# Kernel optimization log

Hardware: AMD Instinct MI355X
Metric: run time of the kernel (lower is better)

The kernel has to match this reference:

```python
import jax, jax.numpy as jnp
import numpy as np

B, S, E = 2, 2048, 2048
H, KVH, D = 16, 4, 128
GROUPS = H // KVH
WINDOW = 1024
CAP = 50.0
ROPE_BASE = 10000.0
RMS_EPS = 1e-6
LN_EPS = 1e-5

def setup_inputs() -> dict:
    key = jax.random.key(0)
    ks = jax.random.split(key, 5)
    return {
        "x": jax.random.normal(ks[0], (B, S, E), jnp.float32),
        "Wq": jax.random.normal(ks[1], (E, E), jnp.float32) * (1.0 / np.sqrt(E)),
        "Wk": jax.random.normal(ks[2], (KVH * D, E), jnp.float32) * (1.0 / np.sqrt(E)),
        "Wv": jax.random.normal(ks[3], (KVH * D, E), jnp.float32) * (1.0 / np.sqrt(E)),
        "Wo": jax.random.normal(ks[4], (E, E), jnp.float32) * (1.0 / np.sqrt(E * H)),
        "q_norm_w": jnp.ones((D,), jnp.float32),
        "k_norm_w": jnp.ones((D,), jnp.float32),
        "ln_gamma": jnp.ones((E,), jnp.float32),
        "ln_beta": jnp.zeros((E,), jnp.float32),
    }

def _rmsnorm(t, w):
    # normalize over last (head) dim
    var = jnp.mean(jnp.square(t), axis=-1, keepdims=True)
    return t * jax.lax.rsqrt(var + RMS_EPS) * w

def _rope(t):
    # t: [B, h, S, D]; rotate-half RoPE
    half = D // 2
    inv_freq = 1.0 / (ROPE_BASE ** (jnp.arange(0, D, 2, dtype=jnp.float32) / D))  # [D/2]
    ang = jnp.arange(S, dtype=jnp.float32)[:, None] * inv_freq[None, :]  # [S, D/2]
    cos = jnp.concatenate([jnp.cos(ang), jnp.cos(ang)], axis=-1)  # [S, D]
    sin = jnp.concatenate([jnp.sin(ang), jnp.sin(ang)], axis=-1)
    t1, t2 = t[..., :half], t[..., half:]
    rot = jnp.concatenate([-t2, t1], axis=-1)
    return t * cos + rot * sin

def reference(x, Wq, Wk, Wv, Wo, q_norm_w, k_norm_w, ln_gamma, ln_beta):
    b, s, _ = x.shape
    q = (x @ Wq.T).reshape(b, s, H, D).transpose(0, 2, 1, 3)    # [B,H,S,D]
    k = (x @ Wk.T).reshape(b, s, KVH, D).transpose(0, 2, 1, 3)  # [B,KVH,S,D]
    v = (x @ Wv.T).reshape(b, s, KVH, D).transpose(0, 2, 1, 3)
    # QK-RMSNorm (Gemma/PaLM2 style), then RoPE
    q = _rope(_rmsnorm(q, q_norm_w))
    k = _rope(_rmsnorm(k, k_norm_w))
    # GQA: repeat KV heads to match query heads
    k = jnp.repeat(k, GROUPS, axis=1)  # [B,H,S,D]
    v = jnp.repeat(v, GROUPS, axis=1)
    scores = jnp.einsum('bhqd,bhkd->bhqk', q, k) / jnp.sqrt(jnp.asarray(D, x.dtype))
    # tanh logit softcap (Gemma2)
    scores = CAP * jnp.tanh(scores / CAP)
    # causal + sliding-window mask: attend to j with 0 <= i-j < WINDOW
    i = jnp.arange(s)[:, None]
    j = jnp.arange(s)[None, :]
    mask = (j <= i) & ((i - j) < WINDOW)  # [S,S]
    neg = jnp.finfo(scores.dtype).min
    scores = jnp.where(mask[None, None], scores, neg)
    attn = jax.nn.softmax(scores, axis=-1)
    out = jnp.einsum('bhqk,bhkd->bhqd', attn, v)  # [B,H,S,D]
    out = out.transpose(0, 2, 1, 3).reshape(b, s, E) @ Wo.T
    # residual + LayerNorm (post-norm)
    y = x + out
    mu = jnp.mean(y, axis=-1, keepdims=True)
    var = jnp.var(y, axis=-1, keepdims=True)
    return (y - mu) * jax.lax.rsqrt(var + LN_EPS) * ln_gamma + ln_beta
```

## Files before the change

### kernel.cpp

```cpp
#include <hip/hip_runtime.h>
#include <stdint.h>

typedef __attribute__((ext_vector_type(8))) short short8;
typedef __attribute__((ext_vector_type(4))) float f32x4;
typedef unsigned short u16;
typedef unsigned int u32;

#define NTOK 4096
#define E 2048
#define S 2048
#define NH 16
#define NKVH 4
#define HD 128
#define NQKV 3072

__device__ __forceinline__ float bf2f(u16 u) {
    return __uint_as_float(((u32)u) << 16);
}
__device__ __forceinline__ u16 f2bf(float f) {
    u32 u = __float_as_uint(f);
    u32 r = (u + 0x7fffu + ((u >> 16) & 1u)) >> 16;
    return (u16)r;
}
__device__ __forceinline__ void gload_lds16(const u16* g, u16* l) {
    __builtin_amdgcn_global_load_lds(
        (const __attribute__((address_space(1))) unsigned int*)(g),
        (__attribute__((address_space(3))) unsigned int*)(l), 16, 0, 0);
}

__global__ void cast5(const float* __restrict__ x, const float* __restrict__ wq,
                      const float* __restrict__ wk, const float* __restrict__ wv,
                      const float* __restrict__ wo,
                      u16* __restrict__ xb, u16* __restrict__ wqkvb,
                      u16* __restrict__ wob) {
    int i = blockIdx.x * 256 + threadIdx.x;
    const float* s; u16* d; int rel;
    if (i < 2097152)      { s = x;  d = xb;  rel = i; }
    else if (i < 3145728) { s = wq; d = wqkvb; rel = i - 2097152; }
    else if (i < 3407872) { s = wk; d = wqkvb + 4194304; rel = i - 3145728; }
    else if (i < 3670016) { s = wv; d = wqkvb + 5242880; rel = i - 3407872; }
    else                  { s = wo; d = wob; rel = i - 3670016; }
    float4 v = *(const float4*)(s + (size_t)rel * 4);
    ushort4 o;
    o.x = f2bf(v.x); o.y = f2bf(v.y); o.z = f2bf(v.z); o.w = f2bf(v.w);
    *(ushort4*)(d + (size_t)rel * 4) = o;
}

#define LADDR(row, ko) ((row) * 64 + ((ko) ^ (((row) & 7) << 3)))
#define GSB   __builtin_amdgcn_sched_barrier(0)
#define GBAR  __builtin_amdgcn_s_barrier()
#define LGKM0 do { asm volatile("s_waitcnt lgkmcnt(0)" ::: "memory"); GSB; } while (0)
#define MIDBAR do { GSB; GBAR; LGKM0; } while (0)
#define ENDBAR do { __builtin_amdgcn_s_setprio(0); GSB; GBAR; } while (0)

__device__ __forceinline__ void stage1(u16* lds, const u16* g, int row0,
                                       int kt, int K, int tid) {
    const int rr = tid >> 3;
    const int chunk = (tid & 7) ^ (rr & 7);
    gload_lds16(g + (size_t)(row0 + rr) * K + kt + chunk * 8,
                lds + (row0 + (tid >> 6) * 8) * 64);
}

__global__ __launch_bounds__(512, 2)
void gemm_qkv(const u16* __restrict__ A, const u16* __restrict__ Bt,
              float* __restrict__ C, int M, int N, int K) {
    __shared__ u16 As2[2 * 8192];
    __shared__ u16 Bs2[2 * 12288];
    const int tid = threadIdx.x;
    const int w = tid >> 6, lane = tid & 63;
    const int lr = lane & 15, quad = lane >> 4;
    const int qo = quad * 8;
    const int wr = w >> 2, wc = w & 3;
    const int am = wr * 64;
    const int bn = wc * 48;

    const int nbx = N / 192;
    int wg = blockIdx.x;
    {
        const int nwg = gridDim.x;
        const int q = nwg >> 3, r = nwg & 7;
        const int xcd = wg & 7, loc = wg >> 3;
        wg = (xcd < r ? xcd * (q + 1) : r * (q + 1) + (xcd - r) * q) + loc;
    }
    const int n0 = (wg % nbx) * 192;
    const int m0 = (wg / nbx) * 128;

    const u16* gA = A + (size_t)m0 * K;
    const u16* gB = Bt + (size_t)n0 * K;
    const int nt = K >> 6;

    f32x4 acc[4][3];
#pragma unroll
    for (int mi = 0; mi < 4; mi++)
#pragma unroll
        for (int ni = 0; ni < 3; ni++)
            acc[mi][ni] = (f32x4){0.f, 0.f, 0.f, 0.f};

    short8 af[4][2], bf[3][2];

    stage1(As2, gA, 0, 0, K, tid);
    stage1(As2, gA, 64, 0, K, tid);
#pragma unroll
    for (int r = 0; r < 3; r++) stage1(Bs2, gB, r * 64, 0, K, tid);
    if (nt > 1) {
        stage1(As2 + 8192, gA, 0, 64, K, tid);
        stage1(As2 + 8192, gA, 64, 64, K, tid);
        stage1(Bs2 + 12288, gB, 0, 64, K, tid);
        stage1(Bs2 + 12288, gB, 64, 64, K, tid);
        asm volatile("s_waitcnt vmcnt(4)" ::: "memory");
    } else {
        asm volatile("s_waitcnt vmcnt(0)" ::: "memory");
    }
    GSB; GBAR;

    for (int t = 0; t < nt; ++t) {
        const int pb = t & 1;
        u16* Ap = As2 + pb * 8192;
        u16* Bp = Bs2 + pb * 12288;
        u16* Bn = Bs2 + (pb ^ 1) * 12288;
        const int kt1 = (t + 1) << 6, kt2 = (t + 2) << 6;

#pragma unroll
        for (int mi = 0; mi < 4; mi++)
#pragma unroll
            for (int kk = 0; kk < 2; kk++)
                af[mi][kk] = *(const short8*)&Ap[LADDR(am + mi * 16 + lr, kk * 32 + qo)];
#pragma unroll
        for (int ni = 0; ni < 3; ni++)
#pragma unroll
            for (int kk = 0; kk < 2; kk++)
                bf[ni][kk] = *(const short8*)&Bp[LADDR(bn + ni * 16 + lr, kk * 32 + qo)];
        if (t + 1 < nt) stage1(Bn, gB, 128, kt1, K, tid);
        GSB; GBAR; LGKM0;
        __builtin_amdgcn_s_setprio(1);
#pragma unroll
        for (int mi = 0; mi < 4; mi++)
#pragma unroll
            for (int ni = 0; ni < 3; ni++)
#pragma unroll
                for (int kk = 0; kk < 2; kk++)
                    acc[mi][ni] = __builtin_amdgcn_mfma_f32_16x16x32_bf16(
                        af[mi][kk], bf[ni][kk], acc[mi][ni], 0, 0, 0);
        __builtin_amdgcn_s_setprio(0);
        if (t + 2 < nt) {
            stage1(Ap, gA, 0, kt2, K, tid);
            stage1(Ap, gA, 64, kt2, K, tid);
            stage1(Bp, gB, 0, kt2, K, tid);
            stage1(Bp, gB, 64, kt2, K, tid);
        }
        if (t + 2 >= nt) {
            asm volatile("s_waitcnt vmcnt(0)" ::: "memory");
        } else {
            asm volatile("s_waitcnt vmcnt(4)" ::: "memory");
        }
        GSB; GBAR;
    }

#pragma unroll
    for (int mi = 0; mi < 4; mi++)
#pragma unroll
        for (int ni = 0; ni < 3; ni++) {
            const int row = m0 + am + mi * 16 + quad * 4;
            const int col = n0 + bn + ni * 16 + lr;
            f32x4 v = acc[mi][ni];
            C[(size_t)(row + 0) * N + col] = v[0];
            C[(size_t)(row + 1) * N + col] = v[1];
            C[(size_t)(row + 2) * N + col] = v[2];
            C[(size_t)(row + 3) * N + col] = v[3];
        }
}

__device__ __forceinline__ void stageA(u16* lds, const u16* g, int ldsrow0,
                                       int g0, int g1, int kt, int K, int tid) {
    const int rr = tid >> 3;
    const int chunk = (tid & 7) ^ (rr & 7);
    const int w8 = (tid >> 6) * 8;
    gload_lds16(g + (size_t)(g0 + rr) * K + kt + chunk * 8,
                lds + (ldsrow0 + w8) * 64);
    gload_lds16(g + (size_t)(g1 + rr) * K + kt + chunk * 8,
                lds + (ldsrow0 + 64 + w8) * 64);
}
__device__ __forceinline__ void stageB(u16* lds, const u16* g, int ldsrow0,
                                       int b0, int b1, int kt, int K, int tid) {
    const int rr = tid >> 3;
    const int grow = (rr & 31) | ((rr & 32) << 1);
    const int chunk = (tid & 7) ^ (rr & 7);
    const int w8 = (tid >> 6) * 8;
    gload_lds16(g + (size_t)(b0 + grow) * K + kt + chunk * 8,
                lds + (ldsrow0 + w8) * 64);
    gload_lds16(g + (size_t)(b1 + grow) * K + kt + chunk * 8,
                lds + (ldsrow0 + 64 + w8) * 64);
}

__global__ __launch_bounds__(512, 2)
void gemm8p(const u16* __restrict__ A, const u16* __restrict__ Bt,
            float* __restrict__ C, int M, int N, int K, int ksz, int nsplit) {
    __shared__ u16 As[2 * 16384];
    __shared__ u16 Bs[2 * 16384];
    const int tid = threadIdx.x;
    const int w = tid >> 6, lane = tid & 63;
    const int lr = lane & 15, quad = lane >> 4;
    const int qo = quad * 8;
    const int wm = (w >> 2) * 128, wn = (w & 3) * 64;
    const int wmh = (w >> 2) * 64, wnq = (w & 3) * 32;

    const int nbx = N >> 8;
    int wg = blockIdx.x;
    {
        const int nwg = gridDim.x;
        const int q = nwg >> 3, r = nwg & 7;
        const int xcd = wg & 7, loc = wg >> 3;
        wg = (xcd < r ? xcd * (q + 1) : r * (q + 1) + (xcd - r) * q) + loc;
    }
    int split = 0;
    if (nsplit == 2) { split = wg & 1; wg >>= 1; }
    const int n0 = (wg % nbx) << 8;
    const int m0 = (wg / nbx) << 8;

    const u16* gA = A + (size_t)m0 * K + split * ksz;
    const u16* gB = Bt + (size_t)n0 * K + split * ksz;
    C += (size_t)split * M * N;
    const int nt = ksz >> 6;

    f32x4 acc[8][4];
#pragma unroll
    for (int mi = 0; mi < 8; mi++)
#pragma unroll
        for (int ni = 0; ni < 4; ni++)
            acc[mi][ni] = (f32x4){0.f, 0.f, 0.f, 0.f};

    short8 alo[4][2], ahi[4][2], blo[2][2], bhi[2][2];

    stageA(As, gA, 0, 0, 128, 0, K, tid);
    stageB(Bs, gB, 0, 0, 128, 0, K, tid);
    stageB(Bs, gB, 128, 32, 160, 0, K, tid);
    stageA(As, gA, 128, 64, 192, 0, K, tid);
    if (nt > 1) {
        stageA(As + 16384, gA, 0, 0, 128, 64, K, tid);
        stageB(Bs + 16384, gB, 0, 0, 128, 64, K, tid);
        stageB(Bs + 16384, gB, 128, 32, 160, 64, K, tid);
        asm volatile("s_waitcnt vmcnt(6)" ::: "memory");
    } else {
        asm volatile("s_waitcnt vmcnt(0)" ::: "memory");
    }
    GSB; GBAR;

    for (int t = 0; t < nt; ++t) {
        const int pb = t & 1;
        u16* Ap = As + pb * 16384;
        u16* Bp = Bs + pb * 16384;
        u16* An = As + (pb ^ 1) * 16384;
        const int kt1 = (t + 1) << 6, kt2 = (t + 2) << 6;

#pragma unroll
        for (int mi = 0; mi < 4; mi++)
#pragma unroll
            for (int kk = 0; kk < 2; kk++)
                alo[mi][kk] = *(const short8*)&Ap[LADDR(wmh + mi * 16 + lr, kk * 32 + qo)];
#pragma unroll
        for (int ni = 0; ni < 2; ni++)
#pragma unroll
            for (int kk = 0; kk < 2; kk++)
                blo[ni][kk] = *(const short8*)&Bp[LADDR(wnq + ni * 16 + lr, kk * 32 + qo)];
        if (t + 1 < nt) stageA(An, gA, 128, 64, 192, kt1, K, tid);
        MIDBAR;
        __builtin_amdgcn_s_setprio(1);
#pragma unroll
        for (int mi = 0; mi < 4; mi++)
#pragma unroll
            for (int ni = 0; ni < 2; ni++)
#pragma unroll
                for (int kk = 0; kk < 2; kk++)
                    acc[mi][ni] = __builtin_amdgcn_mfma_f32_16x16x32_bf16(
                        alo[mi][kk], blo[ni][kk], acc[mi][ni], 0, 0, 0);
        ENDBAR;

#pragma unroll
        for (int ni = 0; ni < 2; ni++)
#pragma unroll
            for (int kk = 0; kk < 2; kk++)
                bhi[ni][kk] = *(const short8*)&Bp[LADDR(128 + wnq + ni * 16 + lr, kk * 32 + qo)];
        if (t + 2 < nt) stageA(Ap, gA, 0, 0, 128, kt2, K, tid);
        MIDBAR;
        __builtin_amdgcn_s_setprio(1);
#pragma unroll
        for (int mi = 0; mi < 4; mi++)
#pragma unroll
            for (int ni = 0; ni < 2; ni++)
#pragma unroll
                for (int kk = 0; kk < 2; kk++)
                    acc[mi][ni + 2] = __builtin_amdgcn_mfma_f32_16x16x32_bf16(
                        alo[mi][kk], bhi[ni][kk], acc[mi][ni + 2], 0, 0, 0);
        ENDBAR;

#pragma unroll
        for (int mi = 0; mi < 4; mi++)
#pragma unroll
            for (int kk = 0; kk < 2; kk++)
                ahi[mi][kk] = *(const short8*)&Ap[LADDR(128 + wmh + mi * 16 + lr, kk * 32 + qo)];
        if (t + 2 < nt) stageB(Bp, gB, 0, 0, 128, kt2, K, tid);
        MIDBAR;
        __builtin_amdgcn_s_setprio(1);
#pragma unroll
        for (int mi = 0; mi < 4; mi++)
#pragma unroll
            for (int ni = 0; ni < 2; ni++)
#pragma unroll
                for (int kk = 0; kk < 2; kk++)
                    acc[mi + 4][ni + 2] = __builtin_amdgcn_mfma_f32_16x16x32_bf16(
                        ahi[mi][kk], bhi[ni][kk], acc[mi + 4][ni + 2], 0, 0, 0);
        ENDBAR;

        if (t + 2 < nt) stageB(Bp, gB, 128, 32, 160, kt2, K, tid);
        __builtin_amdgcn_s_setprio(1);
#pragma unroll
        for (int mi = 0; mi < 4; mi++)
#pragma unroll
            for (int ni = 0; ni < 2; ni++)
#pragma unroll
                for (int kk = 0; kk < 2; kk++)
                    acc[mi + 4][ni] = __builtin_amdgcn_mfma_f32_16x16x32_bf16(
                        ahi[mi][kk], blo[ni][kk], acc[mi + 4][ni], 0, 0, 0);
        __builtin_amdgcn_s_setprio(0);
        if (t + 2 >= nt) {
            asm volatile("s_waitcnt vmcnt(0)" ::: "memory");
        } else {
            asm volatile("s_waitcnt vmcnt(6)" ::: "memory");
        }
        GSB; GBAR;
    }

#pragma unroll
    for (int mi = 0; mi < 8; mi++)
#pragma unroll
        for (int ni = 0; ni < 4; ni++) {
            const int row = m0 + wm + mi * 16 + quad * 4;
            const int col = n0 + wn + ni * 16 + lr;
            f32x4 v = acc[mi][ni];
            C[(size_t)(row + 0) * N + col] = v[0];
            C[(size_t)(row + 1) * N + col] = v[1];
            C[(size_t)(row + 2) * N + col] = v[2];
            C[(size_t)(row + 3) * N + col] = v[3];
        }
}

#define LDT 65
#define RMSBLKS 20480
__global__ __launch_bounds__(256)
void prep(const float* __restrict__ qkv,
          const float* __restrict__ qw, const float* __restrict__ kw,
          u16* __restrict__ qdst, u16* __restrict__ kdst, u16* __restrict__ vdst) {
    __shared__ u16 Ts[128 * LDT];
    if (blockIdx.x < RMSBLKS) {
        int p = blockIdx.x * 4 + (threadIdx.x >> 6);
        int lane = threadIdx.x & 63;
        const float* src; const float* w; u16* dst; int HH;
        if (p < NTOK * NH) { src = qkv; w = qw; dst = qdst; HH = NH; }
        else { p -= NTOK * NH; src = qkv + 2048; w = kw; dst = kdst; HH = NKVH; }
        int n = p / HH;
        int h = p - n * HH;
        int b = n >> 11;
        int s = n & 2047;
        const float* row = src + (size_t)n * NQKV + h * HD;
        float t1 = row[lane];
        float t2 = row[lane + 64];
        float ss = t1 * t1 + t2 * t2;
#pragma unroll
        for (int o = 1; o < 64; o <<= 1) ss += __shfl_xor(ss, o);
        float r = rsqrtf(ss * (1.f / 128.f) + 1e-6f);
        float a1 = t1 * r * w[lane];
        float a2 = t2 * r * w[lane + 64];
        float freq = expf(lane * -0.14391156831212787f);
        float ang = (float)s * freq;
        float sn, cs;
        sincosf(ang, &sn, &cs);
        float o1 = a1 * cs - a2 * sn;
        float o2 = a2 * cs + a1 * sn;
        size_t base = (((size_t)(b * HH + h)) * S + s) * HD;
        dst[base + lane] = f2bf(o1);
        dst[base + 64 + lane] = f2bf(o2);
    } else {
        const int idx = blockIdx.x - RMSBLKS;
        const int t = threadIdx.x;
        const int s0 = (idx & 31) * 64;
        const int kh = (idx >> 5) & 3;
        const int b = idx >> 7;
        const float* base = qkv + ((size_t)(b * S + s0)) * NQKV + 2560 + kh * HD;
#pragma unroll
        for (int i = 0; i < 8; i++) {
            int ii = i * 256 + t;
            int r = ii >> 5, c4 = (ii & 31) * 4;
            float4 v = *(const float4*)(base + (size_t)r * NQKV + c4);
            Ts[(c4 + 0) * LDT + r] = f2bf(v.x);
            Ts[(c4 + 1) * LDT + r] = f2bf(v.y);
            Ts[(c4 + 2) * LDT + r] = f2bf(v.z);
            Ts[(c4 + 3) * LDT + r] = f2bf(v.w);
        }
        __syncthreads();
        u16* obase = vdst + ((size_t)(b * NKVH + kh) * HD) * S + s0;
#pragma unroll
        for (int i = 0; i < 4; i++) {
            int ii = i * 256 + t;
            int d = ii >> 3, s8 = (ii & 7) * 8;
            const u16* row = &Ts[d * LDT + s8];
            short8 o;
#pragma unroll
            for (int j = 0; j < 8; j++) o[j] = (short)row[j];
            *(short8*)(obase + (size_t)d * S + s8) = o;
        }
    }
}

#define KSX(key, cb) ((key) * 128 + ((((cb) ^ ((key) & 15))) * 8))
#define VSX(d, cb)   ((d) * 64 + ((((cb) ^ ((d) & 7))) * 8))
#define PSX(row, cb) ((row) * 64 + ((((cb) ^ ((row) & 7))) * 8))
#define QBLK 64

__global__ __launch_bounds__(256, 4)
void attn_mfma(const u16* __restrict__ qa, const u16* __restrict__ ka,
               const u16* __restrict__ vt, u16* __restrict__ out) {
    __shared__ u16 Ks[64 * 128];
    __shared__ u16 Vs[128 * 64];
    __shared__ u16 Ps[64 * 64];
    const int tid = threadIdx.x;
    const int w = tid >> 6, lane = tid & 63;
    const int lr = lane & 15, quad = lane >> 4;

    const int bid = blockIdx.x;
    const int g = bid >> 8, p = bid & 255;
    const int j = p >> 5, hb = p & 31;
    int qt;
    if (g == 0) qt = 31 - j;
    else if (g == 1) qt = 23 - j;
    else if (g == 2) qt = 8 + j;
    else qt = 7 - j;
    const int h = hb >> 1, b = hb & 1;
    const int kh = h >> 2;
    const int q0 = qt * QBLK;
    const int qg0 = q0 + w * 16;

    const float KQK = 0.0051006974f;
    const float KP  = -144.26950408889634f;

    const u16* kbase0 = ka + (((size_t)(b * NKVH + kh)) * S) * HD;
    const u16* vtbase0 = vt + ((size_t)(b * NKVH + kh) * HD) * S;

    short8 qf[4];
    {
        const u16* qrow = qa + (((size_t)(b * NH + h)) * S + qg0 + lr) * HD;
#pragma unroll
        for (int c = 0; c < 4; c++)
            qf[c] = *(const short8*)(qrow + c * 32 + quad * 8);
    }

    f32x4 O[8];
#pragma unroll
    for (int dt = 0; dt < 8; dt++) O[dt] = (f32x4){0.f, 0.f, 0.f, 0.f};
    float l[4] = {0.f, 0.f, 0.f, 0.f};

    const int jt0 = (q0 >= 1024) ? (q0 - 1024) : 0;
    const int jtend = q0;
    const int qmin = qg0, qmax = qg0 + 15;

    for (int jt = jt0; jt <= jtend; jt += 64) {
        const u16* kbase = kbase0 + (size_t)jt * HD;
        const u16* vtbase = vtbase0 + jt;
        __syncthreads();
#pragma unroll
        for (int i = 0; i < 4; i++) {
            int idx = i * 256 + tid;
            int key = idx >> 4, cbk = (idx & 15) ^ (key & 15);
            gload_lds16(kbase + (size_t)key * HD + cbk * 8,
                        &Ks[(i * 256 + w * 64) * 8]);
            int dd = idx >> 3, cbv = (idx & 7) ^ (dd & 7);
            gload_lds16(vtbase + (size_t)dd * S + cbv * 8,
                        &Vs[(i * 256 + w * 64) * 8]);
        }
        __syncthreads();

        u16* Pw = &Ps[w * 16 * 64];
        bool any = false;

#pragma unroll
        for (int kt = 0; kt < 4; kt++) {
            const int keymin = jt + kt * 16;
            bool need = (keymin <= qmax) && (keymin + 15 >= qmin - 1023);
            bool full = (keymin + 15 <= qmin) && (keymin >= qmax - 1023);
            if (need) {
                any = true;
                f32x4 a = (f32x4){0.f, 0.f, 0.f, 0.f};
                __builtin_amdgcn_s_setprio(1);
#pragma unroll
                for (int c = 0; c < 4; c++) {
                    short8 kf = *(const short8*)(&Ks[KSX(kt * 16 + lr, 4 * c + quad)]);
                    a = __builtin_amdgcn_mfma_f32_16x16x32_bf16(qf[c], kf, a, 0, 0, 0);
                }
                __builtin_amdgcn_s_setprio(0);
#pragma unroll
                for (int r = 0; r < 4; r++) {
                    float t = __builtin_amdgcn_exp2f(a[r] * KQK);
                    float p2 = __builtin_amdgcn_exp2f(
                        KP * __builtin_amdgcn_rcpf(t + 1.f));
                    if (!full) {
                        int rel = keymin + lr - (qg0 + quad * 4 + r);
                        bool valid = (rel <= 0) && (rel > -1024);
                        p2 = valid ? p2 : 0.f;
                    }
                    l[r] += p2;
                    Pw[PSX(quad * 4 + r, kt * 2 + (lr >> 3)) + (lr & 7)] =
                        (u16)(__float_as_uint(p2) >> 16);
                }
            } else {
#pragma unroll
                for (int r = 0; r < 4; r++)
                    Pw[PSX(quad * 4 + r, kt * 2 + (lr >> 3)) + (lr & 7)] = 0;
            }
        }

        if (any) {
            __builtin_amdgcn_s_setprio(1);
#pragma unroll
            for (int c2 = 0; c2 < 2; c2++) {
                short8 pf = *(const short8*)(&Pw[PSX(lr, c2 * 4 + quad)]);
#pragma unroll
                for (int dt = 0; dt < 8; dt++) {
                    short8 vf = *(const short8*)(&Vs[VSX(dt * 16 + lr, c2 * 4 + quad)]);
                    O[dt] = __builtin_amdgcn_mfma_f32_16x16x32_bf16(pf, vf, O[dt], 0, 0, 0);
                }
            }
            __builtin_amdgcn_s_setprio(0);
        }
    }

#pragma unroll
    for (int r = 0; r < 4; r++) {
        l[r] += __shfl_xor(l[r], 1);
        l[r] += __shfl_xor(l[r], 2);
        l[r] += __shfl_xor(l[r], 4);
        l[r] += __shfl_xor(l[r], 8);
    }
#pragma unroll
    for (int r = 0; r < 4; r++) {
        float inv = 1.f / l[r];
        u16* orow = out + ((size_t)(b * S + qg0 + quad * 4 + r)) * E + h * HD;
#pragma unroll
        for (int dt = 0; dt < 8; dt++)
            orow[dt * 16 + lr] = f2bf(O[dt][r] * inv);
    }
}

__global__ __launch_bounds__(256)
void ln_kernel(const float* __restrict__ x, const float* __restrict__ pr,
               const float* __restrict__ pr2,
               const float* __restrict__ g, const float* __restrict__ be,
               float* __restrict__ out) {
    int n = blockIdx.x;
    int tid = threadIdx.x;
    const float* xr = x + (size_t)n * E;
    const float* p = pr + (size_t)n * E;
    const float* p2 = pr2 + (size_t)n * E;
    float y[8];
    float s = 0.f, ss = 0.f;
#pragma unroll
    for (int i = 0; i < 2; i++) {
        float4 a = *(const float4*)(xr + tid * 8 + i * 4);
        float4 b = *(const float4*)(p + tid * 8 + i * 4);
        float4 cc = *(const float4*)(p2 + tid * 8 + i * 4);
        float v0 = a.x + b.x + cc.x, v1 = a.y + b.y + cc.y;
        float v2 = a.z + b.z + cc.z, v3 = a.w + b.w + cc.w;
        y[i * 4 + 0] = v0; y[i * 4 + 1] = v1; y[i * 4 + 2] = v2; y[i * 4 + 3] = v3;
        s += v0 + v1 + v2 + v3;
        ss += v0 * v0 + v1 * v1 + v2 * v2 + v3 * v3;
    }
#pragma unroll
    for (int o = 1; o < 64; o <<= 1) {
        s += __shfl_xor(s, o);
        ss += __shfl_xor(ss, o);
    }
    __shared__ float r0[4], r1[4];
    int w = tid >> 6;
    if ((tid & 63) == 0) { r0[w] = s; r1[w] = ss; }
    __syncthreads();
    s = r0[0] + r0[1] + r0[2] + r0[3];
    ss = r1[0] + r1[1] + r1[2] + r1[3];
    float mu = s * (1.f / 2048.f);
    float var = ss * (1.f / 2048.f) - mu * mu;
    float rs = rsqrtf(var + 1e-5f);
    float* orow = out + (size_t)n * E;
#pragma unroll
    for (int i = 0; i < 8; i++) {
        int c = tid * 8 + i;
        orow[c] = (y[i] - mu) * rs * g[c] + be[c];
    }
}

extern "C" void kernel_launch(void* const* d_in, const int* in_sizes, int n_in,
                              void* d_out, int out_size, void* d_ws, size_t ws_size,
                              hipStream_t stream) {
    (void)in_sizes; (void)n_in; (void)out_size; (void)ws_size;
    const float* x   = (const float*)d_in[0];
    const float* Wq  = (const float*)d_in[1];
    const float* Wk  = (const float*)d_in[2];
    const float* Wv  = (const float*)d_in[3];
    const float* Wo  = (const float*)d_in[4];
    const float* qnw = (const float*)d_in[5];
    const float* knw = (const float*)d_in[6];
    const float* lng = (const float*)d_in[7];
    const float* lnb = (const float*)d_in[8];
    float* out = (float*)d_out;

    char* ws = (char*)d_ws;
    size_t off = 0;
    auto alloc = [&](size_t bytes) -> char* {
        char* pp = ws + off;
        off = (off + bytes + 255) & ~(size_t)255;
        return pp;
    };
    u16*  xb     = (u16*)alloc((size_t)NTOK * E * 2);
    u16*  Wqkvb  = (u16*)alloc((size_t)NQKV * E * 2);
    u16*  Wob    = (u16*)alloc((size_t)E * E * 2);
    float* qkvraw= (float*)alloc((size_t)NTOK * NQKV * 4);
    u16*  qaa    = (u16*)alloc((size_t)NTOK * E * 2);
    u16*  kaa    = (u16*)alloc((size_t)NTOK * 512 * 2);
    u16*  vtt    = (u16*)alloc((size_t)NTOK * 512 * 2);
    u16*  attn_o = xb;
    float* proj  = qkvraw;

    cast5<<<dim3(18432), 256, 0, stream>>>(x, Wq, Wk, Wv, Wo, xb, Wqkvb, Wob);

    gemm_qkv<<<dim3(512), 512, 0, stream>>>(xb, Wqkvb, qkvraw, NTOK, NQKV, E);

    prep<<<dim3(RMSBLKS + 256), 256, 0, stream>>>(qkvraw, qnw, knw, qaa, kaa, vtt);

    attn_mfma<<<dim3(1024), 256, 0, stream>>>(qaa, kaa, vtt, attn_o);

    gemm8p<<<dim3((NTOK / 256) * (E / 256) * 2), 512, 0, stream>>>(
        attn_o, Wob, proj, NTOK, E, E, E / 2, 2);

    ln_kernel<<<dim3(NTOK), 256, 0, stream>>>(
        x, proj, proj + (size_t)NTOK * E, lng, lnb, out);
}
```

Measured before the change: 302.7 us.

## Replace split-K 256x256 output projection GEMM with 128x128 tile kernel

The output projection GEMM moves from a 256x256-tile kernel with split-K of 2 (256 workgroups, two partial fp32 outputs) to a 128x128-tile kernel over the full K (512 workgroups), using the same pipelining as the QKV GEMM. The layernorm kernel now reads one projection buffer instead of summing two partials, which cuts a 32MB write and read of partial results. In exchange the smaller tile lowers data reuse per workgroup and each workgroup runs a longer K loop.

```diff
diff --git a/kernel.cpp b/kernel.cpp
--- a/kernel.cpp
+++ b/kernel.cpp
@@ -50,8 +50,6 @@
 #define GSB   __builtin_amdgcn_sched_barrier(0)
 #define GBAR  __builtin_amdgcn_s_barrier()
 #define LGKM0 do { asm volatile("s_waitcnt lgkmcnt(0)" ::: "memory"); GSB; } while (0)
-#define MIDBAR do { GSB; GBAR; LGKM0; } while (0)
-#define ENDBAR do { __builtin_amdgcn_s_setprio(0); GSB; GBAR; } while (0)
 
 __device__ __forceinline__ void stage1(u16* lds, const u16* g, int row0,
                                        int kt, int K, int tid) {
@@ -170,41 +168,20 @@
         }
 }
 
-__device__ __forceinline__ void stageA(u16* lds, const u16* g, int ldsrow0,
-                                       int g0, int g1, int kt, int K, int tid) {
-    const int rr = tid >> 3;
-    const int chunk = (tid & 7) ^ (rr & 7);
-    const int w8 = (tid >> 6) * 8;
-    gload_lds16(g + (size_t)(g0 + rr) * K + kt + chunk * 8,
-                lds + (ldsrow0 + w8) * 64);
-    gload_lds16(g + (size_t)(g1 + rr) * K + kt + chunk * 8,
-                lds + (ldsrow0 + 64 + w8) * 64);
-}
-__device__ __forceinline__ void stageB(u16* lds, const u16* g, int ldsrow0,
-                                       int b0, int b1, int kt, int K, int tid) {
-    const int rr = tid >> 3;
-    const int grow = (rr & 31) | ((rr & 32) << 1);
-    const int chunk = (tid & 7) ^ (rr & 7);
-    const int w8 = (tid >> 6) * 8;
-    gload_lds16(g + (size_t)(b0 + grow) * K + kt + chunk * 8,
-                lds + (ldsrow0 + w8) * 64);
-    gload_lds16(g + (size_t)(b1 + grow) * K + kt + chunk * 8,
-                lds + (ldsrow0 + 64 + w8) * 64);
-}
-
 __global__ __launch_bounds__(512, 2)
-void gemm8p(const u16* __restrict__ A, const u16* __restrict__ Bt,
-            float* __restrict__ C, int M, int N, int K, int ksz, int nsplit) {
-    __shared__ u16 As[2 * 16384];
-    __shared__ u16 Bs[2 * 16384];
+void gemm_proj(const u16* __restrict__ A, const u16* __restrict__ Bt,
+               float* __restrict__ C, int M, int N, int K) {
+    __shared__ u16 As2[2 * 8192];
+    __shared__ u16 Bs2[2 * 8192];
     const int tid = threadIdx.x;
     const int w = tid >> 6, lane = tid & 63;
     const int lr = lane & 15, quad = lane >> 4;
     const int qo = quad * 8;
-    const int wm = (w >> 2) * 128, wn = (w & 3) * 64;
-    const int wmh = (w >> 2) * 64, wnq = (w & 3) * 32;
-
-    const int nbx = N >> 8;
+    const int wr = w >> 2, wc = w & 3;
+    const int am = wr * 64;
+    const int bn = wc * 32;
+
+    const int nbx = N >> 7;
     int wg = blockIdx.x;
     {
         const int nwg = gridDim.x;
@@ -212,34 +189,31 @@
         const int xcd = wg & 7, loc = wg >> 3;
         wg = (xcd < r ? xcd * (q + 1) : r * (q + 1) + (xcd - r) * q) + loc;
     }
-    int split = 0;
-    if (nsplit == 2) { split = wg & 1; wg >>= 1; }
-    const int n0 = (wg % nbx) << 8;
-    const int m0 = (wg / nbx) << 8;
-
-    const u16* gA = A + (size_t)m0 * K + split * ksz;
-    const u16* gB = Bt + (size_t)n0 * K + split * ksz;
-    C += (size_t)split * M * N;
-    const int nt = ksz >> 6;
-
-    f32x4 acc[8][4];
-#pragma unroll
-    for (int mi = 0; mi < 8; mi++)
-#pragma unroll
-        for (int ni = 0; ni < 4; ni++)
+    const int n0 = (wg % nbx) << 7;
+    const int m0 = (wg / nbx) << 7;
+
+    const u16* gA = A + (size_t)m0 * K;
+    const u16* gB = Bt + (size_t)n0 * K;
+    const int nt = K >> 6;
+
+    f32x4 acc[4][2];
+#pragma unroll
+    for (int mi = 0; mi < 4; mi++)
+#pragma unroll
+        for (int ni = 0; ni < 2; ni++)
             acc[mi][ni] = (f32x4){0.f, 0.f, 0.f, 0.f};
 
-    short8 alo[4][2], ahi[4][2], blo[2][2], bhi[2][2];
-
-    stageA(As, gA, 0, 0, 128, 0, K, tid);
-    stageB(Bs, gB, 0, 0, 128, 0, K, tid);
-    stageB(Bs, gB, 128, 32, 160, 0, K, tid);
-    stageA(As, gA, 128, 64, 192, 0, K, tid);
+    short8 af[4][2], bf[2][2];
+
+    stage1(As2, gA, 0, 0, K, tid);
+    stage1(As2, gA, 64, 0, K, tid);
+    stage1(Bs2, gB, 0, 0, K, tid);
+    stage1(Bs2, gB, 64, 0, K, tid);
     if (nt > 1) {
-        stageA(As + 16384, gA, 0, 0, 128, 64, K, tid);
-        stageB(Bs + 16384, gB, 0, 0, 128, 64, K, tid);
-        stageB(Bs + 16384, gB, 128, 32, 160, 64, K, tid);
-        asm volatile("s_waitcnt vmcnt(6)" ::: "memory");
+        stage1(As2 + 8192, gA, 0, 64, K, tid);
+        stage1(As2 + 8192, gA, 64, 64, K, tid);
+        stage1(Bs2 + 8192, gB, 0, 64, K, tid);
+        asm volatile("s_waitcnt vmcnt(3)" ::: "memory");
     } else {
         asm volatile("s_waitcnt vmcnt(0)" ::: "memory");
     }
@@ -247,23 +221,23 @@
 
     for (int t = 0; t < nt; ++t) {
         const int pb = t & 1;
-        u16* Ap = As + pb * 16384;
-        u16* Bp = Bs + pb * 16384;
-        u16* An = As + (pb ^ 1) * 16384;
+        u16* Ap = As2 + pb * 8192;
+        u16* Bp = Bs2 + pb * 8192;
+        u16* Bn = Bs2 + (pb ^ 1) * 8192;
         const int kt1 = (t + 1) << 6, kt2 = (t + 2) << 6;
 
 #pragma unroll
         for (int mi = 0; mi < 4; mi++)
 #pragma unroll
             for (int kk = 0; kk < 2; kk++)
-                alo[mi][kk] = *(const short8*)&Ap[LADDR(wmh + mi * 16 + lr, kk * 32 + qo)];
+                af[mi][kk] = *(const short8*)&Ap[LADDR(am + mi * 16 + lr, kk * 32 + qo)];
 #pragma unroll
         for (int ni = 0; ni < 2; ni++)
 #pragma unroll
             for (int kk = 0; kk < 2; kk++)
-                blo[ni][kk] = *(const short8*)&Bp[LADDR(wnq + ni * 16 + lr, kk * 32 + qo)];
-        if (t + 1 < nt) stageA(An, gA, 128, 64, 192, kt1, K, tid);
-        MIDBAR;
+                bf[ni][kk] = *(const short8*)&Bp[LADDR(bn + ni * 16 + lr, kk * 32 + qo)];
+        if (t + 1 < nt) stage1(Bn, gB, 64, kt1, K, tid);
+        GSB; GBAR; LGKM0;
         __builtin_amdgcn_s_setprio(1);
 #pragma unroll
         for (int mi = 0; mi < 4; mi++)
@@ -272,70 +246,27 @@
 #pragma unroll
                 for (int kk = 0; kk < 2; kk++)
                     acc[mi][ni] = __builtin_amdgcn_mfma_f32_16x16x32_bf16(
-                        alo[mi][kk], blo[ni][kk], acc[mi][ni], 0, 0, 0);
-        ENDBAR;
-
-#pragma unroll
-        for (int ni = 0; ni < 2; ni++)
-#pragma unroll
-            for (int kk = 0; kk < 2; kk++)
-                bhi[ni][kk] = *(const short8*)&Bp[LADDR(128 + wnq + ni * 16 + lr, kk * 32 + qo)];
-        if (t + 2 < nt) stageA(Ap, gA, 0, 0, 128, kt2, K, tid);
-        MIDBAR;
-        __builtin_amdgcn_s_setprio(1);
-#pragma unroll
-        for (int mi = 0; mi < 4; mi++)
-#pragma unroll
-            for (int ni = 0; ni < 2; ni++)
-#pragma unroll
-                for (int kk = 0; kk < 2; kk++)
-                    acc[mi][ni + 2] = __builtin_amdgcn_mfma_f32_16x16x32_bf16(
-                        alo[mi][kk], bhi[ni][kk], acc[mi][ni + 2], 0, 0, 0);
-        ENDBAR;
-
-#pragma unroll
-        for (int mi = 0; mi < 4; mi++)
-#pragma unroll
-            for (int kk = 0; kk < 2; kk++)
-                ahi[mi][kk] = *(const short8*)&Ap[LADDR(128 + wmh + mi * 16 + lr, kk * 32 + qo)];
-        if (t + 2 < nt) stageB(Bp, gB, 0, 0, 128, kt2, K, tid);
-        MIDBAR;
-        __builtin_amdgcn_s_setprio(1);
-#pragma unroll
-        for (int mi = 0; mi < 4; mi++)
-#pragma unroll
-            for (int ni = 0; ni < 2; ni++)
-#pragma unroll
-                for (int kk = 0; kk < 2; kk++)
-                    acc[mi + 4][ni + 2] = __builtin_amdgcn_mfma_f32_16x16x32_bf16(
-                        ahi[mi][kk], bhi[ni][kk], acc[mi + 4][ni + 2], 0, 0, 0);
-        ENDBAR;
-
-        if (t + 2 < nt) stageB(Bp, gB, 128, 32, 160, kt2, K, tid);
-        __builtin_amdgcn_s_setprio(1);
-#pragma unroll
-        for (int mi = 0; mi < 4; mi++)
-#pragma unroll
-            for (int ni = 0; ni < 2; ni++)
-#pragma unroll
-                for (int kk = 0; kk < 2; kk++)
-                    acc[mi + 4][ni] = __builtin_amdgcn_mfma_f32_16x16x32_bf16(
-                        ahi[mi][kk], blo[ni][kk], acc[mi + 4][ni], 0, 0, 0);
+                        af[mi][kk], bf[ni][kk], acc[mi][ni], 0, 0, 0);
         __builtin_amdgcn_s_setprio(0);
+        if (t + 2 < nt) {
+            stage1(Ap, gA, 0, kt2, K, tid);
+            stage1(Ap, gA, 64, kt2, K, tid);
+            stage1(Bp, gB, 0, kt2, K, tid);
+        }
         if (t + 2 >= nt) {
             asm volatile("s_waitcnt vmcnt(0)" ::: "memory");
         } else {
-            asm volatile("s_waitcnt vmcnt(6)" ::: "memory");
+            asm volatile("s_waitcnt vmcnt(3)" ::: "memory");
         }
         GSB; GBAR;
     }
 
 #pragma unroll
-    for (int mi = 0; mi < 8; mi++)
-#pragma unroll
-        for (int ni = 0; ni < 4; ni++) {
-            const int row = m0 + wm + mi * 16 + quad * 4;
-            const int col = n0 + wn + ni * 16 + lr;
+    for (int mi = 0; mi < 4; mi++)
+#pragma unroll
+        for (int ni = 0; ni < 2; ni++) {
+            const int row = m0 + am + mi * 16 + quad * 4;
+            const int col = n0 + bn + ni * 16 + lr;
             f32x4 v = acc[mi][ni];
             C[(size_t)(row + 0) * N + col] = v[0];
             C[(size_t)(row + 1) * N + col] = v[1];
@@ -551,23 +482,19 @@
 
 __global__ __launch_bounds__(256)
 void ln_kernel(const float* __restrict__ x, const float* __restrict__ pr,
-               const float* __restrict__ pr2,
                const float* __restrict__ g, const float* __restrict__ be,
                float* __restrict__ out) {
     int n = blockIdx.x;
     int tid = threadIdx.x;
     const float* xr = x + (size_t)n * E;
     const float* p = pr + (size_t)n * E;
-    const float* p2 = pr2 + (size_t)n * E;
     float y[8];
     float s = 0.f, ss = 0.f;
 #pragma unroll
     for (int i = 0; i < 2; i++) {
         float4 a = *(const float4*)(xr + tid * 8 + i * 4);
         float4 b = *(const float4*)(p + tid * 8 + i * 4);
-        float4 cc = *(const float4*)(p2 + tid * 8 + i * 4);
-        float v0 = a.x + b.x + cc.x, v1 = a.y + b.y + cc.y;
-        float v2 = a.z + b.z + cc.z, v3 = a.w + b.w + cc.w;
+        float v0 = a.x + b.x, v1 = a.y + b.y, v2 = a.z + b.z, v3 = a.w + b.w;
         y[i * 4 + 0] = v0; y[i * 4 + 1] = v1; y[i * 4 + 2] = v2; y[i * 4 + 3] = v3;
         s += v0 + v1 + v2 + v3;
         ss += v0 * v0 + v1 * v1 + v2 * v2 + v3 * v3;
@@ -634,9 +561,7 @@
 
     attn_mfma<<<dim3(1024), 256, 0, stream>>>(qaa, kaa, vtt, attn_o);
 
-    gemm8p<<<dim3((NTOK / 256) * (E / 256) * 2), 512, 0, stream>>>(
-        attn_o, Wob, proj, NTOK, E, E, E / 2, 2);
-
-    ln_kernel<<<dim3(NTOK), 256, 0, stream>>>(
-        x, proj, proj + (size_t)NTOK * E, lng, lnb, out);
-}
+    gemm_proj<<<dim3(512), 512, 0, stream>>>(attn_o, Wob, proj, NTOK, E, E);
+
+    ln_kernel<<<dim3(NTOK), 256, 0, stream>>>(x, proj, lng, lnb, out);
+}
```

New measurement: 296.0 us. -2.2%, faster.
